# Kernel optimization log

Measured on AMD Instinct MI355X. Metric: run time of the kernel, lower is better.

## Reference

```python
import jax, jax.numpy as jnp
import numpy as np

EPS = 1e-8
NCAND = 24  # 4 verts A + 4 verts B + 16 edge-pair intersections


def _cross(u, v):
    return u[..., 0] * v[..., 1] - u[..., 1] * v[..., 0]


def _get_corners(b):
    # b: [N,5] = (x, z, dx, dz, ry) -> BEV corners [N,4,2] (CCW for positive dims)
    x, z, dx, dz, ry = (b[:, i] for i in range(5))
    c, s = jnp.cos(ry), jnp.sin(ry)
    hx, hz = dx * 0.5, dz * 0.5
    lx = jnp.stack([hx, -hx, -hx, hx], axis=1)
    lz = jnp.stack([hz, hz, -hz, -hz], axis=1)
    cx = lx * c[:, None] - lz * s[:, None] + x[:, None]
    cz = lx * s[:, None] + lz * c[:, None] + z[:, None]
    return jnp.stack([cx, cz], axis=-1)


def _quad_area(C):
    # shoelace area of quad corners [N,4,2]
    nxt = jnp.roll(C, -1, axis=1)
    return 0.5 * jnp.abs(jnp.sum(_cross(C, nxt), axis=1))


def _points_in_quad(P, Q):
    # P: [N,4,2] query points, Q: [N,4,2] convex quad. True if inside (either orientation).
    q1 = Q[:, None, :, :]
    q2 = jnp.roll(Q, -1, axis=1)[:, None, :, :]
    s = _cross(q2 - q1, P[:, :, None, :] - q1)  # [N, 4 pts, 4 edges]
    return jnp.all(s >= -1e-6, axis=-1) | jnp.all(s <= 1e-6, axis=-1)


def _convex_intersect_area(A, B):
    # Area of intersection of two convex quads A,B: [N,4,2].
    N = A.shape[0]
    inA = _points_in_quad(A, B)  # A verts inside B
    inB = _points_in_quad(B, A)  # B verts inside A
    # all 4x4 edge-pair intersections
    a1, a2 = A[:, :, None, :], jnp.roll(A, -1, axis=1)[:, :, None, :]
    b1, b2 = B[:, None, :, :], jnp.roll(B, -1, axis=1)[:, None, :, :]
    da, db = a2 - a1, b2 - b1
    den = _cross(da, db)                       # [N,4,4]
    den_safe = jnp.where(jnp.abs(den) < EPS, 1.0, den)
    t = _cross(b1 - a1, db) / den_safe
    u = _cross(b1 - a1, da) / den_safe
    ok = (jnp.abs(den) >= EPS) & (t >= 0.0) & (t <= 1.0) & (u >= 0.0) & (u <= 1.0)
    ipts = a1 + t[..., None] * da              # [N,4,4,2]
    pts = jnp.concatenate([A, B, ipts.reshape(N, 16, 2)], axis=1)   # [N,24,2]
    mask = jnp.concatenate([inA, inB, ok.reshape(N, 16)], axis=1)   # [N,24]
    cnt = jnp.sum(mask, axis=1)
    ctr = jnp.sum(jnp.where(mask[..., None], pts, 0.0), axis=1) / jnp.maximum(cnt, 1).astype(pts.dtype)[:, None]
    rel = pts - ctr[:, None, :]
    relm = jnp.where(mask[..., None], rel, 1.0)  # avoid atan2(0,0)
    ang = jnp.where(mask, jnp.arctan2(relm[..., 1], relm[..., 0]), 1e9)
    order = jnp.argsort(ang, axis=1)
    rel_s = jnp.take_along_axis(rel, order[..., None], axis=1)       # valid pts first, CCW
    # shoelace over the first cnt points (cyclic)
    contrib = _cross(rel_s, jnp.roll(rel_s, -1, axis=1))             # [N,24]
    idx = jnp.arange(NCAND)[None, :]
    body = jnp.sum(jnp.where(idx < (cnt - 1)[:, None], contrib, 0.0), axis=1)
    li = jnp.broadcast_to(jnp.maximum(cnt - 1, 0)[:, None, None], (N, 1, 2))
    last = jnp.take_along_axis(rel_s, li, axis=1)[:, 0]
    closing = _cross(last, rel_s[:, 0])
    area = 0.5 * jnp.abs(body + closing)
    return jnp.where(cnt >= 3, area, 0.0)


def get_iou3d(pred_bboxes, target_bboxes):
    # Faithful vectorized port of the torch/shapely get_iou3d.
    min_h_a = -(pred_bboxes[:, 1] + pred_bboxes[:, 4] / 2)
    max_h_a = -(pred_bboxes[:, 1] - pred_bboxes[:, 4] / 2)
    min_h_b = -(target_bboxes[:, 1] + target_bboxes[:, 4] / 2)
    max_h_b = -(target_bboxes[:, 1] - target_bboxes[:, 4] / 2)
    h_overlap = jnp.clip(jnp.minimum(max_h_a, max_h_b) - jnp.maximum(min_h_a, min_h_b), 0.0)
    cols = jnp.array([0, 2, 3, 5, 6])
    pa = pred_bboxes[:, cols]
    pb = target_bboxes[:, cols]
    ca = _get_corners(pa)
    cb = _get_corners(pb)
    overlap = _convex_intersect_area(ca, cb)
    overlap3d = overlap * h_overlap
    area_a = _quad_area(ca)
    area_b = _quad_area(cb)
    # NOTE: original code indexes max_h_a[0]-min_h_a[0] (box 0's height) inside the loop;
    # replicated faithfully.
    h_a0 = max_h_a[0] - min_h_a[0]
    union3d = area_a * h_a0 + area_b * (max_h_b - min_h_b) - overlap3d
    return overlap3d / union3d


def setup_inputs() -> dict:
    N = 262144
    key = jax.random.key(0)
    ks = jax.random.split(key, 6)
    # target boxes: [x, y, z, d3, h, d5, ry]
    xz = jax.random.normal(ks[0], (N, 2), jnp.float32) * 20.0
    y = jax.random.normal(ks[1], (N, 1), jnp.float32) * 1.5
    dims = jax.random.uniform(ks[2], (N, 3), jnp.float32, 1.5, 4.5)
    ry = jax.random.uniform(ks[3], (N, 1), jnp.float32, -np.pi, np.pi)
    target = jnp.concatenate([xz[:, :1], y, xz[:, 1:], dims[:, :1], dims[:, 1:2], dims[:, 2:], ry], axis=1)
    noise = jax.random.normal(ks[4], (N, 7), jnp.float32) * jnp.array([0.5, 0.2, 0.5, 0.2, 0.2, 0.2, 0.1], jnp.float32)
    pred = target + noise
    return {"pred_bboxes": pred, "target_bboxes": target}


def reference(pred_bboxes, target_bboxes):
    return get_iou3d(pred_bboxes, target_bboxes)
```

## Files before the change

### kernel.cpp

```cpp
#include <hip/hip_runtime.h>
#include <math.h>

static __device__ __forceinline__ float xprod(float ux, float uz, float vx, float vz) {
    return ux * vz - uz * vx;
}

static __device__ __forceinline__ float edge_contrib(
    const float (&Pxc)[4], const float (&Pzc)[4],
    const float (&Qxc)[4], const float (&Qzc)[4])
{
    float ex[4], ez[4], ec[4];
    #pragma unroll
    for (int j = 0; j < 4; j++) {
        int jn = (j + 1) & 3;
        ex[j] = Qxc[jn] - Qxc[j];
        ez[j] = Qzc[jn] - Qzc[j];
        ec[j] = ex[j] * Qzc[j] - ez[j] * Qxc[j];
    }

    float d[4][4];
    #pragma unroll
    for (int i = 0; i < 4; i++) {
        #pragma unroll
        for (int j = 0; j < 4; j++) {
            d[i][j] = ex[j] * Pzc[i] - ez[j] * Pxc[i] - ec[j];
        }
    }

    float acc = 0.0f;
    #pragma unroll
    for (int i = 0; i < 4; i++) {
        int in_ = (i + 1) & 3;
        float t_lo = 0.0f, t_hi = 1.0f;
        #pragma unroll
        for (int j = 0; j < 4; j++) {
            float d0 = d[i][j], d1 = d[in_][j];
            float den = d0 - d1;
            float t = __fdividef(d0, (den == 0.0f) ? 1.0f : den);
            t_lo = (den < 0.0f) ? fmaxf(t_lo, t) : t_lo;
            t_hi = (den > 0.0f) ? fminf(t_hi, t) : t_hi;
            t_lo = (den == 0.0f && d0 < 0.0f) ? 1e9f : t_lo;
        }
        bool valid = t_lo < t_hi;
        float ax = Pxc[i], az = Pzc[i];
        float dx = Pxc[in_] - ax, dz = Pzc[in_] - az;
        float p0x = ax + t_lo * dx, p0z = az + t_lo * dz;
        float p1x = ax + t_hi * dx, p1z = az + t_hi * dz;
        float c = xprod(p0x, p0z, p1x, p1z);
        acc += valid ? c : 0.0f;
    }
    return acc;
}

__global__ __launch_bounds__(256) void iou3d_kernel(
    const float* __restrict__ pred,
    const float* __restrict__ tgt,
    float* __restrict__ out,
    int N)
{
    int i = blockIdx.x * blockDim.x + threadIdx.x;
    if (i >= N) return;

    const float* pa = pred + (long)i * 7;
    const float* pb = tgt  + (long)i * 7;

    float a_x  = pa[0], a_y = pa[1], a_z = pa[2];
    float a_dx = pa[3], a_dy = pa[4], a_dz = pa[5], a_ry = pa[6];
    float b_x  = pb[0], b_y = pb[1], b_z = pb[2];
    float b_dx = pb[3], b_dy = pb[4], b_dz = pb[5], b_ry = pb[6];

    float min_h_a = -(a_y + a_dy * 0.5f);
    float max_h_a = -(a_y - a_dy * 0.5f);
    float min_h_b = -(b_y + b_dy * 0.5f);
    float max_h_b = -(b_y - b_dy * 0.5f);
    float h_ov = fmaxf(fminf(max_h_a, max_h_b) - fmaxf(min_h_a, min_h_b), 0.0f);

    float y0 = pred[1], dy0 = pred[4];
    float h_a0 = (-(y0 - dy0 * 0.5f)) - (-(y0 + dy0 * 0.5f));

    float mx = 0.5f * (a_x + b_x);
    float mz = 0.5f * (a_z + b_z);
    float ax0 = a_x - mx, az0 = a_z - mz;
    float bx0 = b_x - mx, bz0 = b_z - mz;

    float Axc[4], Azc[4], Bxc[4], Bzc[4];
    {
        float c = __cosf(a_ry), s = __sinf(a_ry);
        float hx = a_dx * 0.5f, hz = a_dz * 0.5f;
        const float lx[4] = { hx, -hx, -hx, hx };
        const float lz[4] = { hz, hz, -hz, -hz };
        #pragma unroll
        for (int k = 0; k < 4; k++) {
            Axc[k] = lx[k] * c - lz[k] * s + ax0;
            Azc[k] = lx[k] * s + lz[k] * c + az0;
        }
    }
    {
        float c = __cosf(b_ry), s = __sinf(b_ry);
        float hx = b_dx * 0.5f, hz = b_dz * 0.5f;
        const float lx[4] = { hx, -hx, -hx, hx };
        const float lz[4] = { hz, hz, -hz, -hz };
        #pragma unroll
        for (int k = 0; k < 4; k++) {
            Bxc[k] = lx[k] * c - lz[k] * s + bx0;
            Bzc[k] = lx[k] * s + lz[k] * c + bz0;
        }
    }

    float area_a = a_dx * a_dz;
    float area_b = b_dx * b_dz;

    float acc = edge_contrib(Axc, Azc, Bxc, Bzc)
              + edge_contrib(Bxc, Bzc, Axc, Azc);
    float area = 0.5f * fabsf(acc);

    float overlap3d = area * h_ov;
    float union3d = area_a * h_a0 + area_b * (max_h_b - min_h_b) - overlap3d;
    out[i] = overlap3d / union3d;
}

extern "C" void kernel_launch(void* const* d_in, const int* in_sizes, int n_in,
                              void* d_out, int out_size, void* d_ws, size_t ws_size,
                              hipStream_t stream) {
    const float* pred = (const float*)d_in[0];
    const float* tgt  = (const float*)d_in[1];
    float* out = (float*)d_out;
    int N = in_sizes[0] / 7;
    int block = 256;
    int grid = (N + block - 1) / block;
    hipLaunchKernelGGL(iou3d_kernel, dim3(grid), dim3(block), 0, stream,
                       pred, tgt, out, N);
}
```

Before: 69.27 us.

## Compute BEV overlap via box-local slab clipping instead of generic edge clipping

Replaces the generic convex-polygon edge clipping (16 edge-plane tests with divisions per direction) with a formulation in box A's local frame. Each box edge is clipped against the other box's axis-aligned slabs using precomputed reciprocals, and the contour-integral terms are evaluated in closed form. This removes most divisions and arithmetic per thread in what is likely an ALU-bound kernel. It relies on infinite or huge reciprocals when edges are axis-parallel, which may give NaN or precision problems in degenerate orientations.

```diff
diff --git a/kernel.cpp b/kernel.cpp
--- a/kernel.cpp
+++ b/kernel.cpp
@@ -1,55 +1,22 @@
 #include <hip/hip_runtime.h>
 #include <math.h>
 
-static __device__ __forceinline__ float xprod(float ux, float uz, float vx, float vz) {
-    return ux * vz - uz * vx;
+static __device__ __forceinline__ float slab_dt(
+    float x0, float z0, float ivx, float ivz, float hx, float hz)
+{
+    float t1 = (-hx - x0) * ivx;
+    float t2 = ( hx - x0) * ivx;
+    float t3 = (-hz - z0) * ivz;
+    float t4 = ( hz - z0) * ivz;
+    float nx = fminf(t1, t2), fx = fmaxf(t1, t2);
+    float nz = fminf(t3, t4), fz = fmaxf(t3, t4);
+    float tlo = fmaxf(fmaxf(nx, nz), 0.0f);
+    float thi = fminf(fminf(fx, fz), 1.0f);
+    return fmaxf(thi - tlo, 0.0f);
 }
 
-static __device__ __forceinline__ float edge_contrib(
-    const float (&Pxc)[4], const float (&Pzc)[4],
-    const float (&Qxc)[4], const float (&Qzc)[4])
-{
-    float ex[4], ez[4], ec[4];
-    #pragma unroll
-    for (int j = 0; j < 4; j++) {
-        int jn = (j + 1) & 3;
-        ex[j] = Qxc[jn] - Qxc[j];
-        ez[j] = Qzc[jn] - Qzc[j];
-        ec[j] = ex[j] * Qzc[j] - ez[j] * Qxc[j];
-    }
-
-    float d[4][4];
-    #pragma unroll
-    for (int i = 0; i < 4; i++) {
-        #pragma unroll
-        for (int j = 0; j < 4; j++) {
-            d[i][j] = ex[j] * Pzc[i] - ez[j] * Pxc[i] - ec[j];
-        }
-    }
-
-    float acc = 0.0f;
-    #pragma unroll
-    for (int i = 0; i < 4; i++) {
-        int in_ = (i + 1) & 3;
-        float t_lo = 0.0f, t_hi = 1.0f;
-        #pragma unroll
-        for (int j = 0; j < 4; j++) {
-            float d0 = d[i][j], d1 = d[in_][j];
-            float den = d0 - d1;
-            float t = __fdividef(d0, (den == 0.0f) ? 1.0f : den);
-            t_lo = (den < 0.0f) ? fmaxf(t_lo, t) : t_lo;
-            t_hi = (den > 0.0f) ? fminf(t_hi, t) : t_hi;
-            t_lo = (den == 0.0f && d0 < 0.0f) ? 1e9f : t_lo;
-        }
-        bool valid = t_lo < t_hi;
-        float ax = Pxc[i], az = Pzc[i];
-        float dx = Pxc[in_] - ax, dz = Pzc[in_] - az;
-        float p0x = ax + t_lo * dx, p0z = az + t_lo * dz;
-        float p1x = ax + t_hi * dx, p1z = az + t_hi * dz;
-        float c = xprod(p0x, p0z, p1x, p1z);
-        acc += valid ? c : 0.0f;
-    }
-    return acc;
+static __device__ __forceinline__ float rcpf(float x) {
+    return __builtin_amdgcn_rcpf(x);
 }
 
 __global__ __launch_bounds__(256) void iou3d_kernel(
@@ -78,41 +45,60 @@
     float y0 = pred[1], dy0 = pred[4];
     float h_a0 = (-(y0 - dy0 * 0.5f)) - (-(y0 + dy0 * 0.5f));
 
-    float mx = 0.5f * (a_x + b_x);
-    float mz = 0.5f * (a_z + b_z);
-    float ax0 = a_x - mx, az0 = a_z - mz;
-    float bx0 = b_x - mx, bz0 = b_z - mz;
+    float ca = __cosf(a_ry), sa = __sinf(a_ry);
+    float cb = __cosf(b_ry), sb = __sinf(b_ry);
+    float c  = cb * ca + sb * sa;
+    float sn = sb * ca - cb * sa;
+    float exw = b_x - a_x, ezw = b_z - a_z;
+    float ox =  ca * exw + sa * ezw;
+    float oz = -sa * exw + ca * ezw;
 
-    float Axc[4], Azc[4], Bxc[4], Bzc[4];
-    {
-        float c = __cosf(a_ry), s = __sinf(a_ry);
-        float hx = a_dx * 0.5f, hz = a_dz * 0.5f;
-        const float lx[4] = { hx, -hx, -hx, hx };
-        const float lz[4] = { hz, hz, -hz, -hz };
-        #pragma unroll
-        for (int k = 0; k < 4; k++) {
-            Axc[k] = lx[k] * c - lz[k] * s + ax0;
-            Azc[k] = lx[k] * s + lz[k] * c + az0;
-        }
-    }
-    {
-        float c = __cosf(b_ry), s = __sinf(b_ry);
-        float hx = b_dx * 0.5f, hz = b_dz * 0.5f;
-        const float lx[4] = { hx, -hx, -hx, hx };
-        const float lz[4] = { hz, hz, -hz, -hz };
-        #pragma unroll
-        for (int k = 0; k < 4; k++) {
-            Bxc[k] = lx[k] * c - lz[k] * s + bx0;
-            Bzc[k] = lx[k] * s + lz[k] * c + bz0;
-        }
-    }
+    float p = 0.5f * a_dx, q = 0.5f * a_dz;
+    float r = 0.5f * b_dx, s = 0.5f * b_dz;
+
+    float ux = r * c,   uz = r * sn;
+    float wx = -s * sn, wz = s * c;
+
+    float B0x = ox + ux + wx, B0z = oz + uz + wz;
+    float B1x = ox - ux + wx, B1z = oz - uz + wz;
+    float B2x = ox - ux - wx, B2z = oz - uz - wz;
+    float B3x = ox + ux - wx, B3z = oz + uz - wz;
+
+    float i_ux = rcpf(ux), i_uz = rcpf(uz);
+    float i_wx = rcpf(wx), i_wz = rcpf(wz);
+
+    float dt0 = slab_dt(B0x, B0z, -0.5f * i_ux, -0.5f * i_uz, p, q);
+    float dt1 = slab_dt(B1x, B1z, -0.5f * i_wx, -0.5f * i_wz, p, q);
+    float dt2 = slab_dt(B2x, B2z,  0.5f * i_ux,  0.5f * i_uz, p, q);
+    float dt3 = slab_dt(B3x, B3z,  0.5f * i_wx,  0.5f * i_wz, p, q);
+
+    float D1 = ox * sn - oz * c;
+    float D2 = ox * c + oz * sn;
+    float rs = r * s;
+    float part1 = 2.0f * (rs * (dt0 + dt1 + dt2 + dt3)
+                        + r * D1 * (dt2 - dt0)
+                        + s * D2 * (dt3 - dt1));
+
+    float Pc = p * c, Psn = p * sn, Qc = q * c, Qsn = q * sn;
+    float i_Pc = rcpf(Pc), i_Psn = rcpf(Psn);
+    float i_Qc = rcpf(Qc), i_Qsn = rcpf(Qsn);
+
+    float fu0 =  Pc + Qsn - D2, fw0 = -Psn + Qc + D1;
+    float fu1 = -Pc + Qsn - D2, fw1 =  Psn + Qc + D1;
+    float fu2 = -Pc - Qsn - D2, fw2 =  Psn - Qc + D1;
+    float fu3 =  Pc - Qsn - D2, fw3 = -Psn - Qc + D1;
+
+    float dA0 = slab_dt(fu0, fw0, -0.5f * i_Pc,   0.5f * i_Psn, r, s);
+    float dA1 = slab_dt(fu1, fw1, -0.5f * i_Qsn, -0.5f * i_Qc,  r, s);
+    float dA2 = slab_dt(fu2, fw2,  0.5f * i_Pc,  -0.5f * i_Psn, r, s);
+    float dA3 = slab_dt(fu3, fw3,  0.5f * i_Qsn,  0.5f * i_Qc,  r, s);
+
+    float part2 = 2.0f * p * q * (dA0 + dA1 + dA2 + dA3);
+
+    float area = 0.5f * fabsf(part1 + part2);
 
     float area_a = a_dx * a_dz;
     float area_b = b_dx * b_dz;
-
-    float acc = edge_contrib(Axc, Azc, Bxc, Bzc)
-              + edge_contrib(Bxc, Bzc, Axc, Azc);
-    float area = 0.5f * fabsf(acc);
 
     float overlap3d = area * h_ov;
     float union3d = area_a * h_a0 + area_b * (max_h_b - min_h_b) - overlap3d;
```

Result: faster. 65.11 us (-6.0%).
